# Optimization experiments

Measured on AMD Instinct MI355X. Metric: run time of the kernel, lower is better.

## Reference

```python
import jax, jax.numpy as jnp
import numpy as np

LAYER_NUM = 2
NUM_CLS = 128
HIDDEN = 256
NUM_NODES = 1024


def setup_inputs() -> dict:
    key = jax.random.key(0)
    ks = jax.random.split(key, 12)
    s = 0.05
    return {
        "x": jax.random.normal(ks[0], (NUM_NODES, HIDDEN), jnp.float32),
        "knowledge": jax.random.uniform(ks[1], (NUM_CLS, NUM_CLS), jnp.float32) / NUM_CLS,
        "w3w": jax.random.normal(ks[2], (HIDDEN, 2 * HIDDEN), jnp.float32) * s,
        "b3w": jax.random.normal(ks[3], (HIDDEN,), jnp.float32) * s,
        "u3": jax.random.normal(ks[4], (HIDDEN, HIDDEN), jnp.float32) * s,
        "bu3": jax.random.normal(ks[5], (HIDDEN,), jnp.float32) * s,
        "w4w": jax.random.normal(ks[6], (HIDDEN, 2 * HIDDEN), jnp.float32) * s,
        "b4w": jax.random.normal(ks[7], (HIDDEN,), jnp.float32) * s,
        "w5w": jax.random.normal(ks[8], (HIDDEN, 2 * HIDDEN), jnp.float32) * s,
        "b5w": jax.random.normal(ks[9], (HIDDEN,), jnp.float32) * s,
        "u5": jax.random.normal(ks[10], (HIDDEN, HIDDEN), jnp.float32) * s,
        "bu5": jax.random.normal(ks[11], (HIDDEN,), jnp.float32) * s,
    }


def reference(x, knowledge, w3w, b3w, u3, bu3, w4w, b4w, w5w, b5w, u5, bu5):
    N, H = x.shape
    C = knowledge.shape[0]
    # hidden[n, c, :] = x[n, :]  (repeat per class)
    hidden = jnp.broadcast_to(x[:, None, :], (N, C, H))
    for _ in range(LAYER_NUM):
        hs = hidden.sum(0)                      # [C, H]
        diff = hs[None, :, :] - hidden          # [N, C, H]
        # knowledge.T @ diff_n  and  knowledge @ diff_n, vectorized over nodes
        left = jnp.einsum('kc,nkh->nch', knowledge, diff)
        right = jnp.einsum('ck,nkh->nch', knowledge, diff)
        av = jnp.concatenate([left, right], axis=-1).reshape(N * C, 2 * H)
        h = hidden.reshape(N * C, H)
        uh3 = h @ u3.T + bu3                    # shared: rv uses fc_eq3_u (source quirk)
        zv = jax.nn.sigmoid(av @ w3w.T + b3w + uh3)
        rv = jax.nn.sigmoid(av @ w4w.T + b4w + uh3)
        hv = jnp.tanh(av @ w5w.T + b5w + (rv * h) @ u5.T + bu5)
        h = (1.0 - zv) * h + zv * hv
        hidden = h.reshape(N, C, H)
    return hidden
```

## Files before the change

### kernel.cpp

```cpp
#include <hip/hip_runtime.h>
#include <cstdint>
#include <cstddef>


#define NODES 1024
#define NCLS  128
#define HID   256

using frag  = __attribute__((ext_vector_type(8))) short;
using frag4 = __attribute__((ext_vector_type(4))) short;
using f32x4 = __attribute__((ext_vector_type(4))) float;

__device__ __forceinline__ float bf2f(unsigned short h){
  unsigned int u = ((unsigned int)h) << 16;
  float f; __builtin_memcpy(&f, &u, 4); return f;
}
__device__ __forceinline__ unsigned short f2bf(float f){
  unsigned int u; __builtin_memcpy(&u, &f, 4);
  u = (u + 0x7fffu + ((u >> 16) & 1u)) >> 16;
  return (unsigned short)u;
}
__device__ __forceinline__ float sigm(float x){ return 1.0f/(1.0f + __expf(-x)); }
__device__ __forceinline__ float tanh_fast(float x){ return 1.0f - 2.0f/(__expf(2.0f*x) + 1.0f); }

#define GLOBAL_AS(p) ((const __attribute__((address_space(1))) void*)(p))
#define LDS_AS(p)    ((__attribute__((address_space(3))) void*)(p))

template<int OUT_BF16>
__global__ __launch_bounds__(256) void gemm_bf16(
    const unsigned short* __restrict__ A0, int ldA0, int K0,
    const unsigned short* __restrict__ A1, int ldA1,
    const unsigned short* __restrict__ BT, int ldB, long bStride,
    void* __restrict__ Cptr, int ldC,
    int Ntiles, int Ktot, unsigned int aMask, int Mtiles)
{
  __shared__ unsigned short As[4096];
  __shared__ unsigned short Bs[4096];
  const int t   = threadIdx.x;
  const int bid = blockIdx.x;
  const int xcd = bid & 7, slot = bid >> 3;
  const int mtPerX = (Mtiles >= 8) ? (Mtiles >> 3) : 1;
  const int mt = xcd * mtPerX + slot / Ntiles;
  const int nt = slot % Ntiles;
  const int lane = t & 63, w = t >> 6;
  const int wm = w >> 1, wn = w & 1;
  const int r = lane & 15, q = lane >> 4;
  const int m0 = mt * 128, n0 = nt * 128;
  const unsigned short* Bbase = BT + (size_t)mt * (size_t)bStride;

  f32x4 acc[4][4] = {};

  for (int kb = 0; kb < Ktot; kb += 32) {
#pragma unroll
    for (int i = 0; i < 2; ++i) {
      int u  = i * 256 + t;
      int mi = u >> 2;
      int kc = (u & 3) * 8;
      int k  = kb + kc;
      const unsigned short* ga;
      if (k < K0) ga = A0 + (size_t)((unsigned int)(m0 + mi) & aMask) * (size_t)ldA0 + k;
      else        ga = A1 + (size_t)(m0 + mi) * (size_t)ldA1 + (k - K0);
      __builtin_amdgcn_global_load_lds(GLOBAL_AS(ga), LDS_AS(&As[u * 8]), 16, 0, 0);
      const unsigned short* gb = Bbase + (size_t)(n0 + mi) * (size_t)ldB + k;
      __builtin_amdgcn_global_load_lds(GLOBAL_AS(gb), LDS_AS(&Bs[u * 8]), 16, 0, 0);
    }
    __syncthreads();

    frag af[4], bf_[4];
#pragma unroll
    for (int x = 0; x < 4; ++x) {
      af[x]  = *(const frag*)&As[(wm * 64 + x * 16 + r) * 32 + q * 8];
      bf_[x] = *(const frag*)&Bs[(wn * 64 + x * 16 + r) * 32 + q * 8];
    }
#pragma unroll
    for (int x = 0; x < 4; ++x)
#pragma unroll
      for (int y = 0; y < 4; ++y)
        acc[x][y] = __builtin_amdgcn_mfma_f32_16x16x32_bf16(af[x], bf_[y], acc[x][y], 0, 0, 0);
    __syncthreads();
  }

#pragma unroll
  for (int x = 0; x < 4; ++x) {
#pragma unroll
    for (int y = 0; y < 4; ++y) {
      int col = n0 + wn * 64 + y * 16 + r;
#pragma unroll
      for (int g = 0; g < 4; ++g) {
        long row = m0 + wm * 64 + x * 16 + q * 4 + g;
        if (OUT_BF16) ((unsigned short*)Cptr)[row * (long)ldC + col] = f2bf(acc[x][y][g]);
        else          ((float*)Cptr)[row * (long)ldC + col] = acc[x][y][g];
      }
    }
  }
}

__global__ __launch_bounds__(256, 4) void gemm_pre(
    const unsigned short* __restrict__ AVH, const unsigned short* __restrict__ H1,
    const unsigned short* __restrict__ WB, unsigned short* __restrict__ PRE)
{
  __shared__ __align__(16) unsigned short SM[16384];
  const int t   = threadIdx.x;
  const int bid = blockIdx.x;
  const int xcd = bid & 7, slot = bid >> 3;
  const int mt = xcd * 128 + slot / 6;
  const int ct = slot % 6;
  const int lane = t & 63, w = t >> 6;
  const int wm = w >> 1, wn = w & 1;
  const int r = lane & 15, q = lane >> 4;
  const int m0 = mt * 128;
  const unsigned short* Wrow = WB + (size_t)(ct * 128) * 768;
  const int nst = (ct < 4) ? 24 : 16;

  f32x4 acc[4][4] = {};

  auto STAGE = [&](int b, int kt) {
    const int kb = kt * 32;
    unsigned short* Asb = SM + b * 4096;
    unsigned short* Bsb = SM + 8192 + b * 4096;
#pragma unroll
    for (int i = 0; i < 2; ++i) {
      int u  = i * 256 + t;
      int mi = u >> 2;
      int gc = (u & 3) ^ ((mi >> 1) & 3);
      const unsigned short* ga;
      if (kb < 512) ga = AVH + (size_t)(m0 + mi) * 512 + kb + gc * 8;
      else          ga = H1  + (size_t)(m0 + mi) * 256 + (kb - 512) + gc * 8;
      __builtin_amdgcn_global_load_lds(GLOBAL_AS(ga), LDS_AS(&Asb[u * 8]), 16, 0, 0);
      __builtin_amdgcn_global_load_lds(GLOBAL_AS(Wrow + (size_t)mi * 768 + kb + gc * 8),
                                       LDS_AS(&Bsb[u * 8]), 16, 0, 0);
    }
  };

  STAGE(0, 0);
  int cur = 0;
  for (int kt = 0; kt < nst; ++kt) {
    if (kt + 1 < nst) {
      STAGE(cur ^ 1, kt + 1);
      asm volatile("s_waitcnt vmcnt(4)" ::: "memory");
    } else {
      asm volatile("s_waitcnt vmcnt(0)" ::: "memory");
    }
    __builtin_amdgcn_s_barrier();
    asm volatile("" ::: "memory");
    const unsigned short* Asb = SM + cur * 4096;
    const unsigned short* Bsb = SM + 8192 + cur * 4096;
    frag af[4], bf_[4];
#pragma unroll
    for (int x = 0; x < 4; ++x) {
      int ra = wm * 64 + x * 16 + r;
      int rb = wn * 64 + x * 16 + r;
      af[x]  = *(const frag*)&Asb[ra * 32 + ((q ^ ((ra >> 1) & 3)) * 8)];
      bf_[x] = *(const frag*)&Bsb[rb * 32 + ((q ^ ((rb >> 1) & 3)) * 8)];
    }
#pragma unroll
    for (int x = 0; x < 4; ++x)
#pragma unroll
      for (int y = 0; y < 4; ++y)
        acc[x][y] = __builtin_amdgcn_mfma_f32_16x16x32_bf16(af[x], bf_[y], acc[x][y], 0, 0, 0);
    asm volatile("" ::: "memory");
    __builtin_amdgcn_s_barrier();
    cur ^= 1;
  }

  unsigned short* L = SM;
#pragma unroll
  for (int x = 0; x < 4; ++x)
#pragma unroll
    for (int y = 0; y < 4; ++y) {
      int j = wn * 64 + y * 16 + r;
#pragma unroll
      for (int g = 0; g < 4; ++g) {
        int c = wm * 64 + x * 16 + q * 4 + g;
        L[c * 128 + (((j >> 3) ^ (c & 12)) * 8) + (j & 7)] = f2bf(acc[x][y][g]);
      }
    }
  __syncthreads();
#pragma unroll
  for (int it = 0; it < 8; ++it) {
    int unit = it * 256 + t;
    int row = unit >> 4, gr = unit & 15;
    frag v = *(const frag*)&L[row * 128 + ((gr ^ (row & 12)) * 8)];
    *(frag*)&PRE[(size_t)(m0 + row) * 768 + ct * 128 + gr * 8] = v;
  }
}

__global__ __launch_bounds__(256, 2) void gemm_l1(
    const float* __restrict__ XW, const float* __restrict__ SW,
    const float* __restrict__ x,
    const float* __restrict__ b3, const float* __restrict__ b4,
    const float* __restrict__ b5, const float* __restrict__ bu3,
    const float* __restrict__ bu5,
    const float* __restrict__ colsum, const float* __restrict__ rowsum,
    const unsigned short* __restrict__ u5b,
    const unsigned short* __restrict__ KTbN, const unsigned short* __restrict__ KbN,
    unsigned short* __restrict__ H1, unsigned short* __restrict__ AVH)
{
  __shared__ unsigned short SM[17408];
  unsigned short* As = SM;
  unsigned short* Bs = SM + 4096;
  unsigned short* L  = SM;
  __shared__ float tP1[256], tP2[256], tP3[256], tX[256];
  __shared__ float tZ1[256], tZ2[256], tZ3[256];
  __shared__ float tV1[256], tV2[256], tV3[256];
  __shared__ float tCS[128], tRS[128];

  const int t = threadIdx.x, bid = blockIdx.x;
  const int xcd = bid & 7, slot = bid >> 3;
  const int n  = xcd * 128 + (slot >> 1);
  const int nt = slot & 1;
  const int lane = t & 63, w = t >> 6, wm = w >> 1, wn = w & 1;
  const int r = lane & 15, q = lane >> 4;
  const int n0 = nt * 128;
  const float* xw = XW + (size_t)n * 1792;

  {
    int i = t;
    float xwi0 = xw[i], xwi1 = xw[256 + i], xwi2 = xw[512 + i], xwi3 = xw[768 + i];
    float xwi4 = xw[1024 + i], xwi5 = xw[1280 + i], xwu = xw[1536 + i];
    tP1[i] = SW[512 + i] - xwi2;
    tP2[i] = SW[768 + i] - xwi3;
    tP3[i] = xwu + b4[i] + bu3[i];
    tX[i]  = x[(size_t)n * HID + i];
    tZ1[i] = SW[i] - xwi0;
    tZ2[i] = SW[256 + i] - xwi1;
    tZ3[i] = xwu + b3[i] + bu3[i];
    tV1[i] = SW[1024 + i] - xwi4;
    tV2[i] = SW[1280 + i] - xwi5;
    tV3[i] = b5[i] + bu5[i];
    if (t < 128) { tCS[t] = colsum[t]; tRS[t] = rowsum[t]; }
  }
  __syncthreads();

  f32x4 acc[4][4] = {};

  for (int kb = 0; kb < 256; kb += 32) {
#pragma unroll
    for (int i = 0; i < 2; ++i) {
      int u  = i * 256 + t;
      int mi = u >> 2;
      int c  = u & 3;
      int k  = kb + c * 8;
      int gc = c ^ ((mi >> 1) & 3);
      __builtin_amdgcn_global_load_lds(GLOBAL_AS(u5b + (size_t)(n0 + mi) * 256 + kb + gc * 8),
                                       LDS_AS(&Bs[u * 8]), 16, 0, 0);
      float cs = tCS[mi], rs = tRS[mi];
      frag a;
#pragma unroll
      for (int e = 0; e < 8; ++e) {
        int i2 = k + e;
        float pre = cs * tP1[i2] + rs * tP2[i2] + tP3[i2];
        a[e] = (short)f2bf(sigm(pre) * tX[i2]);
      }
      *(frag*)&As[mi * 32 + (gc * 8)] = a;
    }
    __syncthreads();

    frag af[4], bf_[4];
#pragma unroll
    for (int xx = 0; xx < 4; ++xx) {
      int ra = wm * 64 + xx * 16 + r;
      int rb = wn * 64 + xx * 16 + r;
      af[xx]  = *(const frag*)&As[ra * 32 + ((q ^ ((ra >> 1) & 3)) * 8)];
      bf_[xx] = *(const frag*)&Bs[rb * 32 + ((q ^ ((rb >> 1) & 3)) * 8)];
    }
#pragma unroll
    for (int xx = 0; xx < 4; ++xx)
#pragma unroll
      for (int y = 0; y < 4; ++y)
        acc[xx][y] = __builtin_amdgcn_mfma_f32_16x16x32_bf16(af[xx], bf_[y], acc[xx][y], 0, 0, 0);
    __syncthreads();
  }

#pragma unroll
  for (int xx = 0; xx < 4; ++xx) {
#pragma unroll
    for (int y = 0; y < 4; ++y) {
      int j = wn * 64 + y * 16 + r;
      int i = n0 + j;
      frag4 pack;
#pragma unroll
      for (int g = 0; g < 4; ++g) {
        int c = wm * 64 + xx * 16 + q * 4 + g;
        float cs = tCS[c], rs = tRS[c];
        float z  = sigm(cs * tZ1[i] + rs * tZ2[i] + tZ3[i]);
        float p5 = cs * tV1[i] + rs * tV2[i] + tV3[i] + acc[xx][y][g];
        float h1 = (1.0f - z) * tX[i] + z * tanh_fast(p5);
        unsigned short hb = f2bf(h1);
        pack[g] = (short)hb;
        H1[(size_t)(n * 128 + c) * HID + i] = hb;
      }
      *(frag4*)&L[j * 136 + (wm * 64 + xx * 16 + q * 4)] = pack;
    }
  }
  __syncthreads();

#pragma unroll 1
  for (int s = 0; s < 2; ++s) {
    const unsigned short* Ks = s ? KbN : KTbN;
#pragma unroll
    for (int xx = 0; xx < 4; ++xx)
#pragma unroll
      for (int y = 0; y < 4; ++y)
        acc[xx][y] = (f32x4){0.0f, 0.0f, 0.0f, 0.0f};
#pragma unroll
    for (int kb = 0; kb < 4; ++kb) {
      frag af[4], bf_[4];
#pragma unroll
      for (int xx = 0; xx < 4; ++xx) {
        int cp = wm * 64 + xx * 16 + r;
        af[xx] = *(const frag*)(Ks + (size_t)cp * 128 + kb * 32 + q * 8);
        int j = wn * 64 + xx * 16 + r;
        bf_[xx] = *(const frag*)&L[j * 136 + kb * 32 + q * 8];
      }
#pragma unroll
      for (int xx = 0; xx < 4; ++xx)
#pragma unroll
        for (int y = 0; y < 4; ++y)
          acc[xx][y] = __builtin_amdgcn_mfma_f32_16x16x32_bf16(af[xx], bf_[y], acc[xx][y], 0, 0, 0);
    }
#pragma unroll
    for (int xx = 0; xx < 4; ++xx)
#pragma unroll
      for (int y = 0; y < 4; ++y) {
        int col = s * 256 + n0 + wn * 64 + y * 16 + r;
#pragma unroll
        for (int g = 0; g < 4; ++g) {
          int cp = wm * 64 + xx * 16 + q * 4 + g;
          AVH[(size_t)(n * 128 + cp) * 512 + col] = f2bf(acc[xx][y][g]);
        }
      }
  }
}

__global__ __launch_bounds__(256) void gemm_l2(
    const unsigned short* __restrict__ PRE, const float* __restrict__ SG,
    const unsigned short* __restrict__ H1, const unsigned short* __restrict__ u5b,
    float* __restrict__ out)
{
  __shared__ unsigned short As[4096], Bs[4096];
  const int t = threadIdx.x, bid = blockIdx.x;
  const int xcd = bid & 7, slot = bid >> 3;
  const int mt = xcd * 128 + (slot >> 1);
  const int nt = slot & 1;
  const int lane = t & 63, w = t >> 6, wm = w >> 1, wn = w & 1;
  const int r = lane & 15, q = lane >> 4;
  const int m0 = mt * 128, n0 = nt * 128;

  f32x4 acc[4][4] = {};

  for (int kb = 0; kb < 256; kb += 32) {
#pragma unroll
    for (int i = 0; i < 2; ++i) {
      int u  = i * 256 + t;
      int mi = u >> 2;
      int c  = u & 3;
      int k  = kb + c * 8;
      int gc = c ^ ((mi >> 1) & 3);
      __builtin_amdgcn_global_load_lds(GLOBAL_AS(u5b + (size_t)(n0 + mi) * 256 + kb + gc * 8),
                                       LDS_AS(&Bs[u * 8]), 16, 0, 0);
      long row = m0 + mi;
      frag p4 = *(const frag*)(PRE + row * 768 + 256 + k);
      frag h1 = *(const frag*)(H1 + row * 256 + k);
      const float* sg = SG + (size_t)mi * 768 + 256 + k;
      frag a;
#pragma unroll
      for (int e = 0; e < 8; ++e) {
        float rv = sigm(sg[e] + bf2f((unsigned short)p4[e]));
        a[e] = (short)f2bf(rv * bf2f((unsigned short)h1[e]));
      }
      *(frag*)&As[mi * 32 + (gc * 8)] = a;
    }
    __syncthreads();

    frag af[4], bf_[4];
#pragma unroll
    for (int xx = 0; xx < 4; ++xx) {
      int ra = wm * 64 + xx * 16 + r;
      int rb = wn * 64 + xx * 16 + r;
      af[xx]  = *(const frag*)&As[ra * 32 + ((q ^ ((ra >> 1) & 3)) * 8)];
      bf_[xx] = *(const frag*)&Bs[rb * 32 + ((q ^ ((rb >> 1) & 3)) * 8)];
    }
#pragma unroll
    for (int xx = 0; xx < 4; ++xx)
#pragma unroll
      for (int y = 0; y < 4; ++y)
        acc[xx][y] = __builtin_amdgcn_mfma_f32_16x16x32_bf16(af[xx], bf_[y], acc[xx][y], 0, 0, 0);
    __syncthreads();
  }

#pragma unroll
  for (int xx = 0; xx < 4; ++xx) {
#pragma unroll
    for (int y = 0; y < 4; ++y) {
      int i = n0 + wn * 64 + y * 16 + r;
#pragma unroll
      for (int g = 0; g < 4; ++g) {
        int c = wm * 64 + xx * 16 + q * 4 + g;
        long row = m0 + c;
        float z  = sigm(SG[(size_t)c * 768 + i] + bf2f(PRE[row * 768 + i]));
        float pv = SG[(size_t)c * 768 + 512 + i] + bf2f(PRE[row * 768 + 512 + i])
                 + acc[xx][y][g];
        float h  = bf2f(H1[row * 256 + i]);
        out[row * 256 + i] = (1.0f - z) * h + z * tanh_fast(pv);
      }
    }
  }
}

__global__ __launch_bounds__(256) void prep_cast(
    const float* __restrict__ x, const float* __restrict__ Kn,
    const float* __restrict__ w3, const float* __restrict__ u3,
    const float* __restrict__ w4, const float* __restrict__ w5,
    const float* __restrict__ u5,
    unsigned short* __restrict__ xb, unsigned short* __restrict__ WB,
    unsigned short* __restrict__ WB2, unsigned short* __restrict__ u5b,
    unsigned short* __restrict__ KbN, unsigned short* __restrict__ KTbN)
{
  int idx = blockIdx.x * 256 + threadIdx.x;
  if (idx < 262144) { xb[idx] = f2bf(x[idx]); return; }
  idx -= 262144;
  if (idx < 589824) {
    int col = idx / 768, j = idx % 768;
    int g = col >> 8, i = col & 255;
    float v;
    if (j < 512) { const float* wg = (g == 0) ? w3 : (g == 1) ? w4 : w5; v = wg[(size_t)i * 512 + j]; }
    else v = (g < 2) ? u3[(size_t)i * 256 + (j - 512)] : 0.0f;
    WB[(size_t)col * 768 + j] = f2bf(v);
    return;
  }
  idx -= 589824;
  if (idx < 458752) {
    int col = idx / 256, h = idx % 256;
    int b = col >> 8, i = col & 255;
    float v = (b < 6) ? ((b < 2 ? w3 : (b < 4 ? w4 : w5))[(size_t)i * 512 + (b & 1) * 256 + h])
                      : u3[(size_t)i * 256 + h];
    WB2[(size_t)col * 256 + h] = f2bf(v);
    return;
  }
  idx -= 458752;
  if (idx < 65536) { u5b[idx] = f2bf(u5[idx]); return; }
  idx -= 65536;
  if (idx < 16384) { int c = idx >> 7, k = idx & 127; KbN[idx]  = f2bf(-Kn[c * 128 + k]); return; }
  idx -= 16384;
  { int c = idx >> 7, k = idx & 127; KTbN[idx] = f2bf(-Kn[k * 128 + c]); }
}

__global__ __launch_bounds__(256) void prep_reduce(
    const float* __restrict__ x, const float* __restrict__ Kn,
    float* __restrict__ S, float* __restrict__ colsum, float* __restrict__ rowsum)
{
  int b = blockIdx.x, t = threadIdx.x;
  if (b < 8) {
    float s = 0.f;
    for (int n = 0; n < 128; ++n) s += x[(size_t)(b * 128 + n) * HID + t];
    atomicAdd(&S[t], s);
  } else if (b == 8) {
    if (t < NCLS) { float s = 0.f; for (int k = 0; k < NCLS; ++k) s += Kn[k * NCLS + t]; colsum[t] = s; }
  } else {
    if (t < NCLS) { float s = 0.f; for (int k = 0; k < NCLS; ++k) s += Kn[t * NCLS + k]; rowsum[t] = s; }
  }
}

__global__ __launch_bounds__(256) void prep_sw(
    const float* __restrict__ S, const float* __restrict__ w3,
    const float* __restrict__ w4, const float* __restrict__ w5, float* __restrict__ SW)
{
  int col = blockIdx.x * 256 + threadIdx.x;
  int b = col >> 8, i = col & 255;
  const float* w = (b < 2) ? w3 : (b < 4) ? w4 : w5;
  const float* row = w + (size_t)i * 512 + (b & 1) * 256;
  float s = 0.f;
  for (int h = 0; h < HID; ++h) s += S[h] * row[h];
  SW[col] = s;
}

__global__ __launch_bounds__(256) void reduce_hs(
    const unsigned short* __restrict__ H1, float* __restrict__ hs)
{
  int bid = blockIdx.x;
  int c = bid >> 5, nch = bid & 31;
  int i = threadIdx.x;
  const unsigned short* p = H1 + (size_t)nch * 32 * NCLS * HID + (size_t)c * HID + i;
  float s = 0.f;
  for (int n = 0; n < 32; ++n) s += bf2f(p[(size_t)n * NCLS * HID]);
  atomicAdd(&hs[c * HID + i], s);
}

__global__ __launch_bounds__(256) void p2a(
    const float* __restrict__ hs, const float* __restrict__ w3,
    const float* __restrict__ w4, const float* __restrict__ w5, float* __restrict__ hsW)
{
  __shared__ float hrow[HID];
  int k = blockIdx.x & 127, b = blockIdx.x >> 7;
  int t = threadIdx.x;
  hrow[t] = hs[k * HID + t];
  __syncthreads();
  const float* w = (b < 2) ? w3 : (b < 4) ? w4 : w5;
  const float* row = w + (size_t)t * 512 + (b & 1) * 256;
  float s = 0.f;
  for (int h = 0; h < HID; ++h) s += hrow[h] * row[h];
  hsW[(size_t)k * 1536 + b * 256 + t] = s;
}

__global__ __launch_bounds__(256) void p2b(
    const float* __restrict__ hsW, const float* __restrict__ Kn,
    const float* __restrict__ b3, const float* __restrict__ b4, const float* __restrict__ b5,
    const float* __restrict__ bu3, const float* __restrict__ bu5, float* __restrict__ SG)
{
  __shared__ float kc[NCLS], kr[NCLS];
  int c = blockIdx.x, t = threadIdx.x;
  if (t < NCLS) { kc[t] = Kn[t * NCLS + c]; kr[t] = Kn[c * NCLS + t]; }
  __syncthreads();
  for (int g = 0; g < 3; ++g) {
    int i = t;
    const float* L = hsW + (size_t)(2 * g) * 256 + i;
    const float* R = hsW + (size_t)(2 * g + 1) * 256 + i;
    float s = 0.f;
    for (int k = 0; k < NCLS; ++k) s += kc[k] * L[(size_t)k * 1536] + kr[k] * R[(size_t)k * 1536];
    const float* bg = (g == 0) ? b3 : (g == 1) ? b4 : b5;
    s += bg[i] + ((g < 2) ? bu3[i] : bu5[i]);
    SG[(size_t)c * 768 + g * 256 + i] = s;
  }
}

extern "C" void kernel_launch(void* const* d_in, const int* in_sizes, int n_in,
                              void* d_out, int out_size, void* d_ws, size_t ws_size,
                              hipStream_t stream) {
  (void)in_sizes; (void)n_in; (void)out_size; (void)ws_size;
  const float* x   = (const float*)d_in[0];
  const float* Kn  = (const float*)d_in[1];
  const float* w3  = (const float*)d_in[2];
  const float* b3  = (const float*)d_in[3];
  const float* u3  = (const float*)d_in[4];
  const float* bu3 = (const float*)d_in[5];
  const float* w4  = (const float*)d_in[6];
  const float* b4  = (const float*)d_in[7];
  const float* w5  = (const float*)d_in[8];
  const float* b5  = (const float*)d_in[9];
  const float* u5  = (const float*)d_in[10];
  const float* bu5 = (const float*)d_in[11];
  float* out = (float*)d_out;

  char* w = (char*)d_ws;
  unsigned short* AVH = (unsigned short*)(w);
  unsigned short* PRE = (unsigned short*)(w + 134217728);
  unsigned short* H1  = (unsigned short*)(w + 335544320);
  float*          XW  = (float*)(w + 402653184);
  char* misc = w + 409993216;
  float* S      = (float*)(misc);
  float* hs     = (float*)(misc + 1024);
  float* SW     = (float*)(misc + 132096);
  float* colsum = (float*)(misc + 138240);
  float* rowsum = (float*)(misc + 138752);
  float* hsW    = (float*)(misc + 139264);
  float* SG     = (float*)(misc + 925696);
  unsigned short* WB   = (unsigned short*)(misc + 1318912);
  unsigned short* WB2  = (unsigned short*)(misc + 2498560);
  unsigned short* u5b  = (unsigned short*)(misc + 3416064);
  unsigned short* KbN  = (unsigned short*)(misc + 3547136);
  unsigned short* KTbN = (unsigned short*)(misc + 3579904);
  unsigned short* xb   = (unsigned short*)(misc + 3612672);

  hipMemsetAsync(misc, 0, 132096, stream);

  prep_cast<<<5504, 256, 0, stream>>>(x, Kn, w3, u3, w4, w5, u5, xb, WB, WB2, u5b, KbN, KTbN);
  prep_reduce<<<10, 256, 0, stream>>>(x, Kn, S, colsum, rowsum);
  prep_sw<<<6, 256, 0, stream>>>(S, w3, w4, w5, SW);

  gemm_bf16<0><<<8 * 14, 256, 0, stream>>>(xb, 256, 256, xb, 256, WB2, 256, 0L,
                                           (void*)XW, 1792, 14, 256, 0xFFFFFFFFu, 8);
  gemm_l1<<<2048, 256, 0, stream>>>(XW, SW, x, b3, b4, b5, bu3, bu5,
                                    colsum, rowsum, u5b, KTbN, KbN, H1, AVH);

  reduce_hs<<<4096, 256, 0, stream>>>(H1, hs);
  p2a<<<768, 256, 0, stream>>>(hs, w3, w4, w5, hsW);
  p2b<<<128, 256, 0, stream>>>(hsW, Kn, b3, b4, b5, bu3, bu5, SG);

  gemm_pre<<<6144, 256, 0, stream>>>(AVH, H1, WB, PRE);

  gemm_l2<<<2048, 256, 0, stream>>>(PRE, SG, H1, u5b, out);
}
```

Measured before the change: 710.8 us.

## Enlarge gemm_pre tiles to 256x256 with 8 waves and phased prefetch

Rewrites the gemm_pre GEMM to use 256x256 output tiles, K=64 steps and 512-thread blocks. Global-to-LDS prefetch of the next K tile is split across four MFMA phases, and s_setprio is raised around the MFMA bursts. The goal is more data reuse per LDS load and better overlap of loads with matrix math. The cost is 128KB of LDS per block, a larger accumulator footprint per thread, and far fewer blocks (1536) to spread across the CUs.

Result: no change. 699.4 us (-1.6%).

```diff
diff --git a/kernel.cpp b/kernel.cpp
--- a/kernel.cpp
+++ b/kernel.cpp
@@ -25,6 +25,7 @@
 
 #define GLOBAL_AS(p) ((const __attribute__((address_space(1))) void*)(p))
 #define LDS_AS(p)    ((__attribute__((address_space(3))) void*)(p))
+#define MFMA16 __builtin_amdgcn_mfma_f32_16x16x32_bf16
 
 template<int OUT_BF16>
 __global__ __launch_bounds__(256) void gemm_bf16(
@@ -76,7 +77,7 @@
     for (int x = 0; x < 4; ++x)
 #pragma unroll
       for (int y = 0; y < 4; ++y)
-        acc[x][y] = __builtin_amdgcn_mfma_f32_16x16x32_bf16(af[x], bf_[y], acc[x][y], 0, 0, 0);
+        acc[x][y] = MFMA16(af[x], bf_[y], acc[x][y], 0, 0, 0);
     __syncthreads();
   }
 
@@ -95,93 +96,126 @@
   }
 }
 
-__global__ __launch_bounds__(256, 4) void gemm_pre(
+__global__ __launch_bounds__(512, 2) void gemm_pre(
     const unsigned short* __restrict__ AVH, const unsigned short* __restrict__ H1,
     const unsigned short* __restrict__ WB, unsigned short* __restrict__ PRE)
 {
-  __shared__ __align__(16) unsigned short SM[16384];
+  __shared__ __align__(16) unsigned short SM[65536];
   const int t   = threadIdx.x;
   const int bid = blockIdx.x;
   const int xcd = bid & 7, slot = bid >> 3;
-  const int mt = xcd * 128 + slot / 6;
-  const int ct = slot % 6;
+  const int mt = xcd * 64 + slot / 3;
+  const int ct = slot % 3;
   const int lane = t & 63, w = t >> 6;
-  const int wm = w >> 1, wn = w & 1;
+  const int wm = w >> 2, wn = w & 3;
   const int r = lane & 15, q = lane >> 4;
-  const int m0 = mt * 128;
-  const unsigned short* Wrow = WB + (size_t)(ct * 128) * 768;
-  const int nst = (ct < 4) ? 24 : 16;
-
-  f32x4 acc[4][4] = {};
-
-  auto STAGE = [&](int b, int kt) {
-    const int kb = kt * 32;
-    unsigned short* Asb = SM + b * 4096;
-    unsigned short* Bsb = SM + 8192 + b * 4096;
-#pragma unroll
-    for (int i = 0; i < 2; ++i) {
-      int u  = i * 256 + t;
-      int mi = u >> 2;
-      int gc = (u & 3) ^ ((mi >> 1) & 3);
-      const unsigned short* ga;
-      if (kb < 512) ga = AVH + (size_t)(m0 + mi) * 512 + kb + gc * 8;
-      else          ga = H1  + (size_t)(m0 + mi) * 256 + (kb - 512) + gc * 8;
-      __builtin_amdgcn_global_load_lds(GLOBAL_AS(ga), LDS_AS(&Asb[u * 8]), 16, 0, 0);
-      __builtin_amdgcn_global_load_lds(GLOBAL_AS(Wrow + (size_t)mi * 768 + kb + gc * 8),
-                                       LDS_AS(&Bsb[u * 8]), 16, 0, 0);
-    }
+  const int m0 = mt * 256;
+  const unsigned short* Wrow = WB + (size_t)(ct * 256) * 768;
+  const int nkt = (ct < 2) ? 12 : 8;
+
+  unsigned short* const Ab0 = SM;
+  unsigned short* const Ab1 = SM + 16384;
+  unsigned short* const Bb0 = SM + 32768;
+  unsigned short* const Bb1 = SM + 49152;
+
+  f32x4 acc[8][4] = {};
+
+  const int smi = t >> 3, sc = t & 7;
+
+  auto ISSUE_A = [&](unsigned short* dst, int kt, int rbase) {
+    int row = rbase + smi;
+    int gc = sc ^ (row & 7);
+    const unsigned short* ga;
+    if (kt < 8) ga = AVH + (size_t)(m0 + row) * 512 + kt * 64 + gc * 8;
+    else        ga = H1  + (size_t)(m0 + row) * 256 + (kt - 8) * 64 + gc * 8;
+    __builtin_amdgcn_global_load_lds(GLOBAL_AS(ga), LDS_AS(&dst[row * 64 + sc * 8]), 16, 0, 0);
   };
-
-  STAGE(0, 0);
-  int cur = 0;
-  for (int kt = 0; kt < nst; ++kt) {
-    if (kt + 1 < nst) {
-      STAGE(cur ^ 1, kt + 1);
-      asm volatile("s_waitcnt vmcnt(4)" ::: "memory");
-    } else {
-      asm volatile("s_waitcnt vmcnt(0)" ::: "memory");
-    }
-    __builtin_amdgcn_s_barrier();
-    asm volatile("" ::: "memory");
-    const unsigned short* Asb = SM + cur * 4096;
-    const unsigned short* Bsb = SM + 8192 + cur * 4096;
-    frag af[4], bf_[4];
-#pragma unroll
-    for (int x = 0; x < 4; ++x) {
-      int ra = wm * 64 + x * 16 + r;
-      int rb = wn * 64 + x * 16 + r;
-      af[x]  = *(const frag*)&Asb[ra * 32 + ((q ^ ((ra >> 1) & 3)) * 8)];
-      bf_[x] = *(const frag*)&Bsb[rb * 32 + ((q ^ ((rb >> 1) & 3)) * 8)];
-    }
-#pragma unroll
-    for (int x = 0; x < 4; ++x)
-#pragma unroll
-      for (int y = 0; y < 4; ++y)
-        acc[x][y] = __builtin_amdgcn_mfma_f32_16x16x32_bf16(af[x], bf_[y], acc[x][y], 0, 0, 0);
-    asm volatile("" ::: "memory");
-    __builtin_amdgcn_s_barrier();
-    cur ^= 1;
-  }
+  auto ISSUE_B = [&](unsigned short* dst, int kt, int rbase) {
+    int row = rbase + smi;
+    int gc = sc ^ (row & 7);
+    __builtin_amdgcn_global_load_lds(GLOBAL_AS(Wrow + (size_t)row * 768 + kt * 64 + gc * 8),
+                                     LDS_AS(&dst[row * 64 + sc * 8]), 16, 0, 0);
+  };
+
+  ISSUE_B(Bb0, 0, 0); ISSUE_B(Bb0, 0, 64); ISSUE_B(Bb0, 0, 128); ISSUE_B(Bb0, 0, 192);
+  ISSUE_A(Ab0, 0, 0); ISSUE_A(Ab0, 0, 128); ISSUE_A(Ab0, 0, 64); ISSUE_A(Ab0, 0, 192);
+  asm volatile("s_waitcnt vmcnt(2)" ::: "memory");
+  __builtin_amdgcn_s_barrier();
+
+#define PRE_PHASE(XG0, ISSUES, TAIL)                                         \
+    {                                                                        \
+      int ra0 = wm * 128 + (XG0) * 16 + r, ra1 = ra0 + 16;                   \
+      frag a00 = *(const frag*)&A[ra0 * 64 + ((q ^ (ra0 & 7)) * 8)];         \
+      frag a01 = *(const frag*)&A[ra0 * 64 + (((4 + q) ^ (ra0 & 7)) * 8)];   \
+      frag a10 = *(const frag*)&A[ra1 * 64 + ((q ^ (ra1 & 7)) * 8)];         \
+      frag a11 = *(const frag*)&A[ra1 * 64 + (((4 + q) ^ (ra1 & 7)) * 8)];   \
+      ISSUES;                                                                \
+      __builtin_amdgcn_s_setprio(1);                                         \
+      _Pragma("unroll")                                                      \
+      for (int y = 0; y < 4; ++y) {                                          \
+        acc[(XG0)][y]     = MFMA16(a00, bf[y][0], acc[(XG0)][y], 0, 0, 0);   \
+        acc[(XG0)][y]     = MFMA16(a01, bf[y][1], acc[(XG0)][y], 0, 0, 0);   \
+        acc[(XG0)+1][y]   = MFMA16(a10, bf[y][0], acc[(XG0)+1][y], 0, 0, 0); \
+        acc[(XG0)+1][y]   = MFMA16(a11, bf[y][1], acc[(XG0)+1][y], 0, 0, 0); \
+      }                                                                      \
+      __builtin_amdgcn_s_setprio(0);                                         \
+      TAIL;                                                                  \
+      asm volatile("" ::: "memory");                                         \
+      __builtin_amdgcn_s_barrier();                                          \
+    }
+
+  for (int kt = 0; kt < nkt; ++kt) {
+    unsigned short* A  = (kt & 1) ? Ab1 : Ab0;
+    unsigned short* B  = (kt & 1) ? Bb1 : Bb0;
+    unsigned short* An = (kt & 1) ? Ab0 : Ab1;
+    unsigned short* Bn = (kt & 1) ? Bb0 : Bb1;
+    const bool more = (kt + 1 < nkt);
+
+    frag bf[4][2];
+#pragma unroll
+    for (int y = 0; y < 4; ++y) {
+      int rb = wn * 64 + y * 16 + r;
+      bf[y][0] = *(const frag*)&B[rb * 64 + ((q ^ (rb & 7)) * 8)];
+      bf[y][1] = *(const frag*)&B[rb * 64 + (((4 + q) ^ (rb & 7)) * 8)];
+    }
+
+    PRE_PHASE(0,
+      { if (more) { ISSUE_B(Bn, kt + 1, 0); ISSUE_B(Bn, kt + 1, 64); } },
+      { })
+    PRE_PHASE(2,
+      { if (more) { ISSUE_B(Bn, kt + 1, 128); ISSUE_B(Bn, kt + 1, 192); } },
+      { if (more) asm volatile("s_waitcnt vmcnt(4)" ::: "memory");
+        else      asm volatile("s_waitcnt vmcnt(0)" ::: "memory"); })
+    PRE_PHASE(4,
+      { if (more) { ISSUE_A(An, kt + 1, 0); ISSUE_A(An, kt + 1, 128); } },
+      { })
+    PRE_PHASE(6,
+      { if (more) { ISSUE_A(An, kt + 1, 64); ISSUE_A(An, kt + 1, 192); } },
+      { if (more) asm volatile("s_waitcnt vmcnt(2)" ::: "memory"); })
+  }
+#undef PRE_PHASE
 
   unsigned short* L = SM;
 #pragma unroll
-  for (int x = 0; x < 4; ++x)
+  for (int xg = 0; xg < 8; ++xg) {
 #pragma unroll
     for (int y = 0; y < 4; ++y) {
       int j = wn * 64 + y * 16 + r;
+      int jc = j >> 3, jl = j & 7;
 #pragma unroll
       for (int g = 0; g < 4; ++g) {
-        int c = wm * 64 + x * 16 + q * 4 + g;
-        L[c * 128 + (((j >> 3) ^ (c & 12)) * 8) + (j & 7)] = f2bf(acc[x][y][g]);
-      }
-    }
+        int c = wm * 128 + xg * 16 + q * 4 + g;
+        L[c * 256 + ((jc ^ (c & 31)) * 8) + jl] = f2bf(acc[xg][y][g]);
+      }
+    }
+  }
   __syncthreads();
 #pragma unroll
-  for (int it = 0; it < 8; ++it) {
-    int unit = it * 256 + t;
-    int row = unit >> 4, gr = unit & 15;
-    frag v = *(const frag*)&L[row * 128 + ((gr ^ (row & 12)) * 8)];
-    *(frag*)&PRE[(size_t)(m0 + row) * 768 + ct * 128 + gr * 8] = v;
+  for (int rr = 0; rr < 16; ++rr) {
+    int unit = rr * 512 + t;
+    int row = unit >> 5, ch = unit & 31;
+    frag v = *(const frag*)&L[row * 256 + ((ch ^ (row & 31)) * 8)];
+    *(frag*)&PRE[(size_t)(m0 + row) * 768 + ct * 256 + ch * 8] = v;
   }
 }
 
@@ -268,7 +302,7 @@
     for (int xx = 0; xx < 4; ++xx)
 #pragma unroll
       for (int y = 0; y < 4; ++y)
-        acc[xx][y] = __builtin_amdgcn_mfma_f32_16x16x32_bf16(af[xx], bf_[y], acc[xx][y], 0, 0, 0);
+        acc[xx][y] = MFMA16(af[xx], bf_[y], acc[xx][y], 0, 0, 0);
     __syncthreads();
   }
 
@@ -317,7 +351,7 @@
       for (int xx = 0; xx < 4; ++xx)
 #pragma unroll
         for (int y = 0; y < 4; ++y)
-          acc[xx][y] = __builtin_amdgcn_mfma_f32_16x16x32_bf16(af[xx], bf_[y], acc[xx][y], 0, 0, 0);
+          acc[xx][y] = MFMA16(af[xx], bf_[y], acc[xx][y], 0, 0, 0);
     }
 #pragma unroll
     for (int xx = 0; xx < 4; ++xx)
@@ -385,7 +419,7 @@
     for (int xx = 0; xx < 4; ++xx)
 #pragma unroll
       for (int y = 0; y < 4; ++y)
-        acc[xx][y] = __builtin_amdgcn_mfma_f32_16x16x32_bf16(af[xx], bf_[y], acc[xx][y], 0, 0, 0);
+        acc[xx][y] = MFMA16(af[xx], bf_[y], acc[xx][y], 0, 0, 0);
     __syncthreads();
   }
 
@@ -577,7 +611,7 @@
   p2a<<<768, 256, 0, stream>>>(hs, w3, w4, w5, hsW);
   p2b<<<128, 256, 0, stream>>>(hsW, Kn, b3, b4, b5, bu3, bu5, SG);
 
-  gemm_pre<<<6144, 256, 0, stream>>>(AVH, H1, WB, PRE);
+  gemm_pre<<<1536, 512, 0, stream>>>(AVH, H1, WB, PRE);
 
   gemm_l2<<<2048, 256, 0, stream>>>(PRE, SG, H1, u5b, out);
 }
```
